# Kernel optimization log

Measured on AMD Instinct MI355X. Metric: run time of the kernel, lower is better.

## Reference

```python
import jax, jax.numpy as jnp
import numpy as np

B, N, DIM, H, DH = 2, 2048, 512, 8, 64
INNER = H * DH  # == DIM, required by the q.view trick in the original module
STEP = 4


def setup_inputs() -> dict:
    key = jax.random.key(0)
    k1, k2, k3 = jax.random.split(key, 3)
    x = jax.random.normal(k1, (B, N, DIM), jnp.float32)
    # to_qkv: Linear(dim, 4*inner_dim, bias=False); stored as [in, out] for x @ W
    W_qkv = jax.random.normal(k2, (DIM, 4 * INNER), jnp.float32) * 0.02
    # to_out: Linear(2*inner_dim, dim) with bias
    W_out = jax.random.normal(k3, (2 * INNER, DIM), jnp.float32) * 0.02
    b_out = jnp.zeros((DIM,), jnp.float32)
    return {"x": x, "W_qkv": W_qkv, "W_out": W_out, "b_out": b_out}


def reference(x, W_qkv, W_out, b_out):
    b, n, _ = x.shape
    h, dh = H, DH
    scale = dh ** -0.5

    qkvt = x @ W_qkv                       # [b, n, 4*inner]
    q, k, v, t = jnp.split(qkvt, 4, axis=-1)
    to_heads = lambda z: z.reshape(b, n, h, dh).transpose(0, 2, 1, 3)  # [b,h,n,dh]
    q, k, v, t = map(to_heads, (q, k, v, t))

    # pad q by repeating its last row yushu times (note: yushu=4 when n%4==0)
    yushu = STEP - n % STEP
    q = jnp.concatenate([q, jnp.repeat(q[:, :, -1:, :], yushu, axis=2)], axis=2)
    q0 = q.reshape(b, h, STEP, (n + yushu) // STEP, dh)[:, :, 0]  # [b,h,(n+yushu)/4,dh]
    q = jnp.tile(q0, (1, 1, STEP, 1))[:, :, :n]                   # [b,h,n,dh]

    dots = jnp.einsum('bhnd,bhmd->bhnm', q, k) * scale
    attn1 = jax.nn.softmax(dots, axis=-1)

    # fixed distance-decay attention: exp(-|i-j|/e), column-normalized
    pos = jnp.arange(1, n + 1, dtype=x.dtype)
    tg = jnp.abs(pos[None, :] - pos[:, None])                     # [n, n]
    attn2 = jnp.exp(-tg / jnp.exp(jnp.asarray(1.0, x.dtype)))
    # torch: attn2 / attn2.sum(-1) broadcasts [n] over last axis (divides column j by row-sum j)
    attn2 = attn2 / attn2.sum(-1)

    out1 = jnp.einsum('bhnm,bhmd->bhnd', attn1, v)
    out2 = jnp.einsum('nm,bhmd->bhnd', attn2, t)  # attn2 shared across b,h; no repeat needed
    out = jnp.concatenate([out1, out2], axis=-1)   # [b,h,n,2*dh]
    out = out.transpose(0, 2, 1, 3).reshape(b, n, 2 * h * dh)  # b n (h d)
    return out @ W_out + b_out  # dropout=0.0 -> identity
```

## Files before the change

kernel.cpp:

```cpp
#include <hip/hip_runtime.h>

#define NSEQ 2048
#define NB   2
#define NH   8

typedef unsigned short u16;
typedef __attribute__((ext_vector_type(8))) short s8v;
typedef __attribute__((ext_vector_type(4))) float f4v;

static __device__ __forceinline__ u16 f2bf(float f) {
  unsigned u = __float_as_uint(f);
  unsigned r = (u + 0x7fffu + ((u >> 16) & 1u)) >> 16;
  return (u16)r;
}
static __device__ __forceinline__ unsigned pk2(float a, float b) {
  return (unsigned)f2bf(a) | ((unsigned)f2bf(b) << 16);
}
static __device__ __forceinline__ float bf2f(u16 v) {
  return __uint_as_float(((unsigned)v) << 16);
}

typedef __attribute__((address_space(3))) unsigned int lds_u32;
typedef const __attribute__((address_space(1))) unsigned int glob_u32;
static __device__ __forceinline__ void load16(const void* g, void* l) {
  __builtin_amdgcn_global_load_lds((glob_u32*)g, (lds_u32*)l, 16, 0, 0);
}

__global__ __launch_bounds__(256)
void prep_kernel(const float* __restrict__ x, const float* __restrict__ Wqkv,
                 const float* __restrict__ Wout, u16* __restrict__ xb,
                 u16* __restrict__ WqkvT, u16* __restrict__ W1hi, u16* __restrict__ W1lo,
                 u16* __restrict__ W2hi, u16* __restrict__ W2lo) {
  __shared__ float tile[32][33];
  const int bid = blockIdx.x;
  if (bid < 1024) {
    long i = ((long)bid * 256 + threadIdx.x) * 8;
    float4 a = *(const float4*)&x[i];
    float4 b = *(const float4*)&x[i + 4];
    uint4 w;
    w.x = pk2(a.x, a.y); w.y = pk2(a.z, a.w);
    w.z = pk2(b.x, b.y); w.w = pk2(b.z, b.w);
    *(uint4*)&xb[i] = w;
    return;
  }
  const int tx = threadIdx.x & 31, ty = threadIdx.x >> 5;
  if (bid < 2048) {
    int b2 = bid - 1024;
    int c0 = (b2 & 63) * 32, r0 = (b2 >> 6) * 32;
#pragma unroll
    for (int s = 0; s < 32; s += 8)
      tile[ty + s][tx] = Wqkv[(long)(r0 + ty + s) * 2048 + c0 + tx];
    __syncthreads();
#pragma unroll
    for (int s = 0; s < 32; s += 8)
      WqkvT[(long)(c0 + ty + s) * 512 + r0 + tx] = f2bf(tile[tx][ty + s]);
    return;
  }
  {
    int b3 = bid - 2048;
    int part = b3 >= 256;
    if (part) b3 -= 256;
    u16* hi = part ? W2hi : W1hi;
    u16* lo = part ? W2lo : W1lo;
    int c0 = (b3 & 15) * 32, r0 = (b3 >> 4) * 32;
#pragma unroll
    for (int s = 0; s < 32; s += 8) {
      int k = r0 + ty + s;
      int srcrow = ((k >> 6) * 128) + part * 64 + (k & 63);
      tile[ty + s][tx] = Wout[(long)srcrow * 512 + c0 + tx];
    }
    __syncthreads();
#pragma unroll
    for (int s = 0; s < 32; s += 8) {
      float v = tile[tx][ty + s];
      u16 h = f2bf(v);
      float rem = v - bf2f(h);
      long o = (long)(c0 + ty + s) * 512 + r0 + tx;
      hi[o] = h;
      lo[o] = f2bf(rem);
    }
  }
}

__global__ __launch_bounds__(256)
void gemm1_fused(const u16* __restrict__ xb, const u16* __restrict__ WqkvT,
                 u16* __restrict__ qkvtb, u16* __restrict__ qu) {
  const int bx = blockIdx.x, by = blockIdx.y;
  const bool isq = bx >= 12;
  if (isq && by >= 9) return;
  __shared__ alignas(16) u16 As[128 * 32];
  __shared__ alignas(16) u16 Bs[128 * 32];
  const int tid = threadIdx.x, lane = tid & 63, wave = tid >> 6;
  const int l15 = lane & 15, quad = lane >> 4;
  const int wr = wave >> 1, wc = wave & 1;
  const int Brow0 = isq ? (bx - 12) * 128 : 512 + bx * 128;

  f4v acc[4][4];
#pragma unroll
  for (int i = 0; i < 4; ++i)
#pragma unroll
    for (int j = 0; j < 4; ++j) acc[i][j] = (f4v){0.f, 0.f, 0.f, 0.f};

  for (int k0 = 0; k0 < 512; k0 += 32) {
    __syncthreads();
#pragma unroll
    for (int c = 0; c < 2; ++c) {
      int off = (c * 4 + wave) * 1024 + lane * 16;
      int r = off >> 6, cb = (off & 63) >> 1;
      int gar;
      if (!isq) {
        gar = by * 128 + r;
      } else {
        int rr = by * 128 + r;
        int b = rr >= 576;
        int s = rr - (b ? 576 : 0);
        if (s >= 513) s -= 513;
        gar = b * 2048 + s;
      }
      load16(&xb[(long)gar * 512 + k0 + cb], ((char*)As) + off);
      load16(&WqkvT[(long)(Brow0 + r) * 512 + k0 + cb], ((char*)Bs) + off);
    }
    __syncthreads();

    s8v bf[4];
#pragma unroll
    for (int j = 0; j < 4; ++j)
      bf[j] = *(const s8v*)&Bs[(wc * 64 + j * 16 + l15) * 32 + quad * 8];
#pragma unroll
    for (int i = 0; i < 4; ++i) {
      s8v af = *(const s8v*)&As[(wr * 64 + i * 16 + l15) * 32 + quad * 8];
#pragma unroll
      for (int j = 0; j < 4; ++j)
        acc[i][j] = __builtin_amdgcn_mfma_f32_16x16x32_bf16(af, bf[j], acc[i][j], 0, 0, 0);
    }
  }

#pragma unroll
  for (int i = 0; i < 4; ++i)
#pragma unroll
    for (int rr = 0; rr < 4; ++rr) {
      int row = by * 128 + wr * 64 + i * 16 + quad * 4 + rr;
#pragma unroll
      for (int j = 0; j < 4; ++j) {
        int col = wc * 64 + j * 16 + l15;
        u16 v = f2bf(acc[i][j][rr]);
        if (!isq)
          qkvtb[(long)row * 2048 + 512 + bx * 128 + col] = v;
        else
          qu[(long)row * 512 + (bx - 12) * 128 + col] = v;
      }
    }
}

template<int BM, int BN, int TI, int TJ, bool BSPLIT, bool BIAS, bool OUTBF, bool ADDG1>
__global__ __launch_bounds__(256)
void gemm_bt_bf16(const u16* __restrict__ A, const u16* __restrict__ Bhi,
                  const u16* __restrict__ Blo, const float* __restrict__ bias,
                  const float* __restrict__ G1, void* __restrict__ Cout,
                  int M, int N, int K) {
  __shared__ alignas(16) u16 As[BM * 32];
  __shared__ alignas(16) u16 Bs[BN * 32];
  __shared__ alignas(16) u16 Bs2[BSPLIT ? BN * 32 : 8];
  const int tid = threadIdx.x, lane = tid & 63, wave = tid >> 6;
  const int l15 = lane & 15, quad = lane >> 4;
  const int wr = wave >> 1, wc = wave & 1;
  const long m0 = (long)blockIdx.y * BM, n0 = (long)blockIdx.x * BN;

  f4v acc[TI][TJ];
#pragma unroll
  for (int i = 0; i < TI; ++i)
#pragma unroll
    for (int j = 0; j < TJ; ++j) acc[i][j] = (f4v){0.f, 0.f, 0.f, 0.f};

  for (int k0 = 0; k0 < K; k0 += 32) {
    __syncthreads();
#pragma unroll
    for (int c = 0; c < BM / 64; ++c) {
      int off = (c * 4 + wave) * 1024 + lane * 16;
      int r = off >> 6, cb = (off & 63) >> 1;
      load16(&A[(m0 + r) * K + k0 + cb], ((char*)As) + off);
    }
#pragma unroll
    for (int c = 0; c < BN / 64; ++c) {
      int off = (c * 4 + wave) * 1024 + lane * 16;
      int r = off >> 6, cb = (off & 63) >> 1;
      load16(&Bhi[(n0 + r) * K + k0 + cb], ((char*)Bs) + off);
      if constexpr (BSPLIT)
        load16(&Blo[(n0 + r) * K + k0 + cb], ((char*)Bs2) + off);
    }
    __syncthreads();

    s8v bf[TJ], bf2[BSPLIT ? TJ : 1];
#pragma unroll
    for (int j = 0; j < TJ; ++j) {
      bf[j] = *(const s8v*)&Bs[(wc * (TJ * 16) + j * 16 + l15) * 32 + quad * 8];
      if constexpr (BSPLIT)
        bf2[j] = *(const s8v*)&Bs2[(wc * (TJ * 16) + j * 16 + l15) * 32 + quad * 8];
    }
#pragma unroll
    for (int i = 0; i < TI; ++i) {
      s8v af = *(const s8v*)&As[(wr * (TI * 16) + i * 16 + l15) * 32 + quad * 8];
#pragma unroll
      for (int j = 0; j < TJ; ++j) {
        acc[i][j] = __builtin_amdgcn_mfma_f32_16x16x32_bf16(af, bf[j], acc[i][j], 0, 0, 0);
        if constexpr (BSPLIT)
          acc[i][j] = __builtin_amdgcn_mfma_f32_16x16x32_bf16(af, bf2[j], acc[i][j], 0, 0, 0);
      }
    }
  }

#pragma unroll
  for (int i = 0; i < TI; ++i)
#pragma unroll
    for (int rr = 0; rr < 4; ++rr) {
      long row = m0 + wr * (TI * 16) + i * 16 + quad * 4 + rr;
      long g1row = 0;
      if constexpr (ADDG1)
        g1row = (long)((int)(row >> 11) * 576 + ((int)(row & 2047) % 513)) * 512;
#pragma unroll
      for (int j = 0; j < TJ; ++j) {
        long col = n0 + wc * (TJ * 16) + j * 16 + l15;
        float v = acc[i][j][rr];
        if constexpr (BIAS) v += bias[col];
        if constexpr (ADDG1) v += G1[g1row + col];
        if constexpr (OUTBF)
          ((u16*)Cout)[row * N + col] = f2bf(v);
        else
          ((float*)Cout)[row * N + col] = v;
      }
    }
}

__global__ __launch_bounds__(256)
void attn_kernel(const u16* __restrict__ qkvt, const u16* __restrict__ qu,
                 float* __restrict__ Opart, float* __restrict__ rspart) {
  __shared__ alignas(16) u16 Qs[64][72];
  __shared__ alignas(16) u16 Ks[64][72];
  __shared__ alignas(16) u16 Vt[64][72];
  __shared__ alignas(16) float Ps[4][16][68];

  const int tid  = threadIdx.x;
  const int lane = tid & 63, wave = tid >> 6;
  const int l15  = lane & 15, quad = lane >> 4;
  const int qtile = blockIdx.x;
  const int bh = blockIdx.y;
  const int split = blockIdx.z;
  const int b = bh >> 3, h = bh & 7;
  const long rowbase = (long)b * NSEQ;

#pragma unroll
  for (int p = 0; p < 2; ++p) {
    int chunk = tid + p * 256;
    int row = chunk >> 3, cc = chunk & 7;
    int eff = (qtile * 64 + row) % 513;
    *(uint4*)&Qs[row][cc * 8] =
        *(const uint4*)&qu[((long)(b * 576 + eff)) * 512 + h * 64 + cc * 8];
  }
  __syncthreads();

  s8v qf[2];
  {
    const int mrow = wave * 16 + l15;
    qf[0] = *(const s8v*)&Qs[mrow][quad * 8];
    qf[1] = *(const s8v*)&Qs[mrow][32 + quad * 8];
  }

  f4v oacc[4];
#pragma unroll
  for (int i = 0; i < 4; ++i) oacc[i] = (f4v){0.f, 0.f, 0.f, 0.f};
  float rs[4] = {0.f, 0.f, 0.f, 0.f};

  for (int kt = 0; kt < 8; ++kt) {
    __syncthreads();
    const int kb = split * 512 + kt * 64;
#pragma unroll
    for (int p = 0; p < 2; ++p) {
      int chunk = tid + p * 256;
      int row = chunk >> 3, cc = chunk & 7;
      *(uint4*)&Ks[row][cc * 8] =
          *(const uint4*)&qkvt[(rowbase + kb + row) * 2048 + 512 + h * 64 + cc * 8];
    }
    {
      const int d = tid & 63;
      const int w0 = (tid >> 6) * 16;
#pragma unroll
      for (int p = 0; p < 2; ++p) {
        int j8 = w0 + p * 8;
        unsigned vv[8];
#pragma unroll
        for (int rj = 0; rj < 8; ++rj)
          vv[rj] = qkvt[(rowbase + kb + j8 + rj) * 2048 + 1024 + h * 64 + d];
        uint4 w;
        w.x = vv[0] | (vv[1] << 16); w.y = vv[2] | (vv[3] << 16);
        w.z = vv[4] | (vv[5] << 16); w.w = vv[6] | (vv[7] << 16);
        *(uint4*)&Vt[d][j8] = w;
      }
    }
    __syncthreads();

#pragma unroll
    for (int nt = 0; nt < 4; ++nt) {
      f4v s = {0.f, 0.f, 0.f, 0.f};
      s8v kf0 = *(const s8v*)&Ks[nt * 16 + l15][quad * 8];
      s8v kf1 = *(const s8v*)&Ks[nt * 16 + l15][32 + quad * 8];
      s = __builtin_amdgcn_mfma_f32_16x16x32_bf16(qf[0], kf0, s, 0, 0, 0);
      s = __builtin_amdgcn_mfma_f32_16x16x32_bf16(qf[1], kf1, s, 0, 0, 0);
#pragma unroll
      for (int rr = 0; rr < 4; ++rr) {
        float p = __expf(s[rr] * 0.125f);
        rs[rr] += p;
        Ps[wave][quad * 4 + rr][nt * 16 + l15] = p;
      }
    }
    asm volatile("" ::: "memory");

    s8v pf[2];
#pragma unroll
    for (int f = 0; f < 2; ++f) {
      const float* pr = &Ps[wave][l15][f * 32 + quad * 8];
      float4 p0 = *(const float4*)pr;
      float4 p1 = *(const float4*)(pr + 4);
      uint4 w;
      w.x = pk2(p0.x, p0.y); w.y = pk2(p0.z, p0.w);
      w.z = pk2(p1.x, p1.y); w.w = pk2(p1.z, p1.w);
      pf[f] = __builtin_bit_cast(s8v, w);
    }
#pragma unroll
    for (int nt = 0; nt < 4; ++nt) {
      s8v vf0 = *(const s8v*)&Vt[nt * 16 + l15][quad * 8];
      s8v vf1 = *(const s8v*)&Vt[nt * 16 + l15][32 + quad * 8];
      oacc[nt] = __builtin_amdgcn_mfma_f32_16x16x32_bf16(pf[0], vf0, oacc[nt], 0, 0, 0);
      oacc[nt] = __builtin_amdgcn_mfma_f32_16x16x32_bf16(pf[1], vf1, oacc[nt], 0, 0, 0);
    }
  }

  const long sb = ((long)split * 16 + bh) * 576;
#pragma unroll
  for (int rr = 0; rr < 4; ++rr) {
    float t = rs[rr];
    t += __shfl_xor(t, 1);
    t += __shfl_xor(t, 2);
    t += __shfl_xor(t, 4);
    t += __shfl_xor(t, 8);
    int row = qtile * 64 + wave * 16 + quad * 4 + rr;
    if (l15 == 0) rspart[sb + row] = t;
#pragma unroll
    for (int nt = 0; nt < 4; ++nt)
      Opart[(sb + row) * 64 + nt * 16 + l15] = oacc[nt][rr];
  }
}

__global__ __launch_bounds__(256)
void attn_combine(const float* __restrict__ Opart, const float* __restrict__ rspart,
                  u16* __restrict__ O1u) {
  int idx = blockIdx.x * 256 + threadIdx.x;
  int d4 = idx & 15, rowbh = idx >> 4;
  int bh = rowbh / 576, row = rowbh - bh * 576;
  int b = bh >> 3, h = bh & 7;
  float4 o = {0.f, 0.f, 0.f, 0.f};
  float rsum = 0.f;
#pragma unroll
  for (int s = 0; s < 4; ++s) {
    long base = ((long)s * 16 + bh) * 576 + row;
    float4 v = *(const float4*)&Opart[base * 64 + d4 * 4];
    o.x += v.x; o.y += v.y; o.z += v.z; o.w += v.w;
    rsum += rspart[base];
  }
  float inv = 1.0f / rsum;
  unsigned w0 = pk2(o.x * inv, o.y * inv);
  unsigned w1 = pk2(o.z * inv, o.w * inv);
  uint2 w = {w0, w1};
  *(uint2*)&O1u[((long)(b * 576 + row)) * 512 + h * 64 + d4 * 4] = w;
}

__global__ __launch_bounds__(256)
void out2_kernel(const u16* __restrict__ qkvt, u16* __restrict__ O2) {
  __shared__ u16 Ts[256 * 64];
  __shared__ float Is[256];
  const int tid = threadIdx.x;
  const int rg = blockIdx.x;
  const int bh = blockIdx.y;
  const int b = bh >> 3, h = bh & 7;
  const int g0 = rg * 64 - 96;
#pragma unroll
  for (int c = 0; c < 8; ++c) {
    int chunk = c * 256 + tid;
    int row = chunk >> 3, cc = chunk & 7;
    int gr = g0 + row;
    uint4 w = {0u, 0u, 0u, 0u};
    if (gr >= 0 && gr < NSEQ)
      w = *(const uint4*)&qkvt[((long)(b * NSEQ + gr)) * 2048 + 1536 + h * 64 + cc * 8];
    *(uint4*)&Ts[row * 64 + cc * 8] = w;
  }
  {
    const float ie = 0.36787944117144233f;
    const float rr = 0.69220062755534635f;
    const float inv1mr = 1.0f / (1.0f - rr);
    int gr = g0 + tid;
    float val = 0.f;
    if (gr >= 0 && gr < NSEQ) {
      float rj = __expf(-ie * (float)gr);
      float rn = __expf(-ie * (float)(NSEQ - 1 - gr));
      float s = 1.0f + (rr - rr * rj) * inv1mr + (rr - rr * rn) * inv1mr;
      val = 1.0f / s;
    }
    Is[tid] = val;
  }
  __syncthreads();

  const int d = tid & 63, sub = tid >> 6;
  const float r = 0.69220062755534635f;
  const int lo = 96 + sub * 16;
  float F = 0.f;
  float Fv[16];
#pragma unroll 8
  for (int j = lo - 96; j < lo; ++j)
    F = F * r + Is[j] * bf2f(Ts[j * 64 + d]);
#pragma unroll
  for (int k = 0; k < 16; ++k) {
    int j = lo + k;
    F = F * r + Is[j] * bf2f(Ts[j * 64 + d]);
    Fv[k] = F;
  }
  float G = 0.f;
#pragma unroll 8
  for (int j = lo + 15 + 96; j > lo + 15; --j)
    G = G * r + Is[j] * bf2f(Ts[j * 64 + d]);
#pragma unroll
  for (int k = 15; k >= 0; --k) {
    int j = lo + k;
    float u = Is[j] * bf2f(Ts[j * 64 + d]);
    G = G * r + u;
    O2[((long)(b * NSEQ + g0 + j)) * 512 + h * 64 + d] = f2bf(Fv[k] + G - u);
  }
}

extern "C" void kernel_launch(void* const* d_in, const int* in_sizes, int n_in,
                              void* d_out, int out_size, void* d_ws, size_t ws_size,
                              hipStream_t stream) {
  (void)in_sizes; (void)n_in; (void)out_size; (void)ws_size;
  const float* x    = (const float*)d_in[0];
  const float* Wqkv = (const float*)d_in[1];
  const float* Wout = (const float*)d_in[2];
  const float* bout = (const float*)d_in[3];
  float* out = (float*)d_out;

  u16*   qkvtb = (u16*)d_ws;
  u16*   qu    = qkvtb + (size_t)4096 * 2048;
  u16*   O2    = qu    + (size_t)1152 * 512;
  u16*   O1u   = O2    + (size_t)4096 * 512;
  u16*   xb    = O1u   + (size_t)1152 * 512;
  u16*   WqkvT = xb    + (size_t)4096 * 512;
  u16*   W1hi  = WqkvT + (size_t)2048 * 512;
  u16*   W1lo  = W1hi  + (size_t)512 * 512;
  u16*   W2hi  = W1lo  + (size_t)512 * 512;
  u16*   W2lo  = W2hi  + (size_t)512 * 512;
  float* Opart = (float*)(W2lo + (size_t)512 * 512);
  float* rsp   = Opart + (size_t)4 * 16 * 576 * 64;
  float* G1    = Opart;

  prep_kernel<<<dim3(2560), 256, 0, stream>>>(x, Wqkv, Wout, xb, WqkvT,
                                              W1hi, W1lo, W2hi, W2lo);
  gemm1_fused<<<dim3(16, 32), 256, 0, stream>>>(xb, WqkvT, qkvtb, qu);
  attn_kernel<<<dim3(9, 16, 4), 256, 0, stream>>>(qkvtb, qu, Opart, rsp);
  attn_combine<<<dim3(576), 256, 0, stream>>>(Opart, rsp, O1u);
  out2_kernel<<<dim3(32, 16), 256, 0, stream>>>(qkvtb, O2);
  gemm_bt_bf16<128, 64, 4, 2, true, false, false, false>
      <<<dim3(8, 9), 256, 0, stream>>>(O1u, W1hi, W1lo, nullptr, nullptr,
                                       G1, 1152, 512, 512);
  gemm_bt_bf16<128, 64, 4, 2, true, true, false, true>
      <<<dim3(8, 32), 256, 0, stream>>>(O2, W2hi, W2lo, bout, G1,
                                        out, 4096, 512, 512);
}
```

Before: 146.3 us.

## Write V pre-transposed from QKV GEMM, store P as bf16, drop W_out lo split

The QKV GEMM epilogue now writes the V projection into a head-major transposed buffer, so the attention kernel can load V tiles with coalesced 16-byte reads instead of strided scalar gathers. The attention probabilities are converted to bf16 when stored to LDS, which halves the LDS footprint and removes the reload-and-pack step. The output-projection GEMMs no longer use the hi/lo bf16 split of W_out, which removes an extra weight stream and extra MFMA work at some cost in precision.

```diff
diff --git a/kernel.cpp b/kernel.cpp
--- a/kernel.cpp
+++ b/kernel.cpp
@@ -29,8 +29,8 @@
 __global__ __launch_bounds__(256)
 void prep_kernel(const float* __restrict__ x, const float* __restrict__ Wqkv,
                  const float* __restrict__ Wout, u16* __restrict__ xb,
-                 u16* __restrict__ WqkvT, u16* __restrict__ W1hi, u16* __restrict__ W1lo,
-                 u16* __restrict__ W2hi, u16* __restrict__ W2lo) {
+                 u16* __restrict__ WqkvT, u16* __restrict__ W1hi,
+                 u16* __restrict__ W2hi) {
   __shared__ float tile[32][33];
   const int bid = blockIdx.x;
   if (bid < 1024) {
@@ -61,7 +61,6 @@
     int part = b3 >= 256;
     if (part) b3 -= 256;
     u16* hi = part ? W2hi : W1hi;
-    u16* lo = part ? W2lo : W1lo;
     int c0 = (b3 & 15) * 32, r0 = (b3 >> 4) * 32;
 #pragma unroll
     for (int s = 0; s < 32; s += 8) {
@@ -72,19 +71,16 @@
     __syncthreads();
 #pragma unroll
     for (int s = 0; s < 32; s += 8) {
-      float v = tile[tx][ty + s];
-      u16 h = f2bf(v);
-      float rem = v - bf2f(h);
       long o = (long)(c0 + ty + s) * 512 + r0 + tx;
-      hi[o] = h;
-      lo[o] = f2bf(rem);
+      hi[o] = f2bf(tile[tx][ty + s]);
     }
   }
 }
 
 __global__ __launch_bounds__(256)
 void gemm1_fused(const u16* __restrict__ xb, const u16* __restrict__ WqkvT,
-                 u16* __restrict__ qkvtb, u16* __restrict__ qu) {
+                 u16* __restrict__ qkvtb, u16* __restrict__ qu,
+                 u16* __restrict__ VtG) {
   const int bx = blockIdx.x, by = blockIdx.y;
   const bool isq = bx >= 12;
   if (isq && by >= 9) return;
@@ -135,21 +131,37 @@
     }
   }
 
-#pragma unroll
-  for (int i = 0; i < 4; ++i)
-#pragma unroll
-    for (int rr = 0; rr < 4; ++rr) {
-      int row = by * 128 + wr * 64 + i * 16 + quad * 4 + rr;
+  const bool isv = (!isq) && bx >= 4 && bx < 8;
+#pragma unroll
+  for (int i = 0; i < 4; ++i) {
+    int row0 = by * 128 + wr * 64 + i * 16 + quad * 4;
+    if (isv) {
+      int b = row0 >> 11, n = row0 & 2047;
 #pragma unroll
       for (int j = 0; j < 4; ++j) {
-        int col = wc * 64 + j * 16 + l15;
-        u16 v = f2bf(acc[i][j][rr]);
-        if (!isq)
-          qkvtb[(long)row * 2048 + 512 + bx * 128 + col] = v;
-        else
-          qu[(long)row * 512 + (bx - 12) * 128 + col] = v;
-      }
-    }
+        int vcol = (bx - 4) * 128 + wc * 64 + j * 16 + l15;
+        int h = vcol >> 6, d = vcol & 63;
+        uint2 w;
+        w.x = pk2(acc[i][j][0], acc[i][j][1]);
+        w.y = pk2(acc[i][j][2], acc[i][j][3]);
+        *(uint2*)&VtG[(((long)b * 8 + h) * 64 + d) * 2048 + n] = w;
+      }
+    } else {
+#pragma unroll
+      for (int rr = 0; rr < 4; ++rr) {
+        int row = row0 + rr;
+#pragma unroll
+        for (int j = 0; j < 4; ++j) {
+          int col = wc * 64 + j * 16 + l15;
+          u16 v = f2bf(acc[i][j][rr]);
+          if (!isq)
+            qkvtb[(long)row * 2048 + 512 + bx * 128 + col] = v;
+          else
+            qu[(long)row * 512 + (bx - 12) * 128 + col] = v;
+        }
+      }
+    }
+  }
 }
 
 template<int BM, int BN, int TI, int TJ, bool BSPLIT, bool BIAS, bool OUTBF, bool ADDG1>
@@ -233,11 +245,12 @@
 
 __global__ __launch_bounds__(256)
 void attn_kernel(const u16* __restrict__ qkvt, const u16* __restrict__ qu,
-                 float* __restrict__ Opart, float* __restrict__ rspart) {
+                 const u16* __restrict__ VtG, float* __restrict__ Opart,
+                 float* __restrict__ rspart) {
   __shared__ alignas(16) u16 Qs[64][72];
   __shared__ alignas(16) u16 Ks[64][72];
   __shared__ alignas(16) u16 Vt[64][72];
-  __shared__ alignas(16) float Ps[4][16][68];
+  __shared__ alignas(16) u16 Ps[4][16][72];
 
   const int tid  = threadIdx.x;
   const int lane = tid & 63, wave = tid >> 6;
@@ -247,6 +260,7 @@
   const int split = blockIdx.z;
   const int b = bh >> 3, h = bh & 7;
   const long rowbase = (long)b * NSEQ;
+  const long vtbase = ((long)b * 8 + h) * 64 * 2048;
 
 #pragma unroll
   for (int p = 0; p < 2; ++p) {
@@ -279,22 +293,8 @@
       int row = chunk >> 3, cc = chunk & 7;
       *(uint4*)&Ks[row][cc * 8] =
           *(const uint4*)&qkvt[(rowbase + kb + row) * 2048 + 512 + h * 64 + cc * 8];
-    }
-    {
-      const int d = tid & 63;
-      const int w0 = (tid >> 6) * 16;
-#pragma unroll
-      for (int p = 0; p < 2; ++p) {
-        int j8 = w0 + p * 8;
-        unsigned vv[8];
-#pragma unroll
-        for (int rj = 0; rj < 8; ++rj)
-          vv[rj] = qkvt[(rowbase + kb + j8 + rj) * 2048 + 1024 + h * 64 + d];
-        uint4 w;
-        w.x = vv[0] | (vv[1] << 16); w.y = vv[2] | (vv[3] << 16);
-        w.z = vv[4] | (vv[5] << 16); w.w = vv[6] | (vv[7] << 16);
-        *(uint4*)&Vt[d][j8] = w;
-      }
+      *(uint4*)&Vt[row][cc * 8] =
+          *(const uint4*)&VtG[vtbase + (long)row * 2048 + kb + cc * 8];
     }
     __syncthreads();
 
@@ -309,28 +309,19 @@
       for (int rr = 0; rr < 4; ++rr) {
         float p = __expf(s[rr] * 0.125f);
         rs[rr] += p;
-        Ps[wave][quad * 4 + rr][nt * 16 + l15] = p;
+        Ps[wave][quad * 4 + rr][nt * 16 + l15] = f2bf(p);
       }
     }
     asm volatile("" ::: "memory");
 
-    s8v pf[2];
-#pragma unroll
-    for (int f = 0; f < 2; ++f) {
-      const float* pr = &Ps[wave][l15][f * 32 + quad * 8];
-      float4 p0 = *(const float4*)pr;
-      float4 p1 = *(const float4*)(pr + 4);
-      uint4 w;
-      w.x = pk2(p0.x, p0.y); w.y = pk2(p0.z, p0.w);
-      w.z = pk2(p1.x, p1.y); w.w = pk2(p1.z, p1.w);
-      pf[f] = __builtin_bit_cast(s8v, w);
-    }
+    s8v pf0 = *(const s8v*)&Ps[wave][l15][quad * 8];
+    s8v pf1 = *(const s8v*)&Ps[wave][l15][32 + quad * 8];
 #pragma unroll
     for (int nt = 0; nt < 4; ++nt) {
       s8v vf0 = *(const s8v*)&Vt[nt * 16 + l15][quad * 8];
       s8v vf1 = *(const s8v*)&Vt[nt * 16 + l15][32 + quad * 8];
-      oacc[nt] = __builtin_amdgcn_mfma_f32_16x16x32_bf16(pf[0], vf0, oacc[nt], 0, 0, 0);
-      oacc[nt] = __builtin_amdgcn_mfma_f32_16x16x32_bf16(pf[1], vf1, oacc[nt], 0, 0, 0);
+      oacc[nt] = __builtin_amdgcn_mfma_f32_16x16x32_bf16(pf0, vf0, oacc[nt], 0, 0, 0);
+      oacc[nt] = __builtin_amdgcn_mfma_f32_16x16x32_bf16(pf1, vf1, oacc[nt], 0, 0, 0);
     }
   }
 
@@ -447,28 +438,26 @@
 
   u16*   qkvtb = (u16*)d_ws;
   u16*   qu    = qkvtb + (size_t)4096 * 2048;
-  u16*   O2    = qu    + (size_t)1152 * 512;
+  u16*   VtG   = qu    + (size_t)1152 * 512;
+  u16*   O2    = VtG   + (size_t)2 * 8 * 64 * 2048;
   u16*   O1u   = O2    + (size_t)4096 * 512;
   u16*   xb    = O1u   + (size_t)1152 * 512;
   u16*   WqkvT = xb    + (size_t)4096 * 512;
   u16*   W1hi  = WqkvT + (size_t)2048 * 512;
-  u16*   W1lo  = W1hi  + (size_t)512 * 512;
-  u16*   W2hi  = W1lo  + (size_t)512 * 512;
-  u16*   W2lo  = W2hi  + (size_t)512 * 512;
-  float* Opart = (float*)(W2lo + (size_t)512 * 512);
+  u16*   W2hi  = W1hi  + (size_t)512 * 512;
+  float* Opart = (float*)(W2hi + (size_t)512 * 512);
   float* rsp   = Opart + (size_t)4 * 16 * 576 * 64;
   float* G1    = Opart;
 
-  prep_kernel<<<dim3(2560), 256, 0, stream>>>(x, Wqkv, Wout, xb, WqkvT,
-                                              W1hi, W1lo, W2hi, W2lo);
-  gemm1_fused<<<dim3(16, 32), 256, 0, stream>>>(xb, WqkvT, qkvtb, qu);
-  attn_kernel<<<dim3(9, 16, 4), 256, 0, stream>>>(qkvtb, qu, Opart, rsp);
+  prep_kernel<<<dim3(2560), 256, 0, stream>>>(x, Wqkv, Wout, xb, WqkvT, W1hi, W2hi);
+  gemm1_fused<<<dim3(16, 32), 256, 0, stream>>>(xb, WqkvT, qkvtb, qu, VtG);
+  attn_kernel<<<dim3(9, 16, 4), 256, 0, stream>>>(qkvtb, qu, VtG, Opart, rsp);
   attn_combine<<<dim3(576), 256, 0, stream>>>(Opart, rsp, O1u);
   out2_kernel<<<dim3(32, 16), 256, 0, stream>>>(qkvtb, O2);
-  gemm_bt_bf16<128, 64, 4, 2, true, false, false, false>
-      <<<dim3(8, 9), 256, 0, stream>>>(O1u, W1hi, W1lo, nullptr, nullptr,
+  gemm_bt_bf16<128, 64, 4, 2, false, false, false, false>
+      <<<dim3(8, 9), 256, 0, stream>>>(O1u, W1hi, nullptr, nullptr, nullptr,
                                        G1, 1152, 512, 512);
-  gemm_bt_bf16<128, 64, 4, 2, true, true, false, true>
-      <<<dim3(8, 32), 256, 0, stream>>>(O2, W2hi, W2lo, bout, G1,
+  gemm_bt_bf16<128, 64, 4, 2, false, true, false, true>
+      <<<dim3(8, 32), 256, 0, stream>>>(O2, W2hi, nullptr, bout, G1,
                                         out, 4096, 512, 512);
 }
```

Result: faster. 142.2 us (-2.8%).
